# Kernel tuning notes

Measured on AMD Instinct MI355X. Metric: run time of the kernel, lower is better.

The kernel has to match this reference:

```python
import jax, jax.numpy as jnp
import numpy as np

N_NODES = 50000
N_EDGES = 800000
IN_DIM = 128
ATT_DIM = 128
NEG_SLOPE = 0.01  # nn.LeakyReLU default


def setup_inputs() -> dict:
    key = jax.random.key(0)
    ks = jax.random.split(key, 8)
    x = jax.random.normal(ks[0], (N_NODES, IN_DIM), dtype=jnp.float32)
    src_idx = jax.random.randint(ks[1], (N_EDGES,), 0, N_NODES, dtype=jnp.int32)
    dst_idx = jax.random.randint(ks[2], (N_EDGES,), 0, N_NODES, dtype=jnp.int32)
    # small init scale keeps exp(score) numerically tame
    src_w = jax.random.normal(ks[3], (IN_DIM, ATT_DIM), dtype=jnp.float32) * 0.05
    src_b = jnp.zeros((ATT_DIM,), dtype=jnp.float32)
    dst_w = jax.random.normal(ks[4], (IN_DIM, ATT_DIM), dtype=jnp.float32) * 0.05
    dst_b = jnp.zeros((ATT_DIM,), dtype=jnp.float32)
    att_w = jax.random.normal(ks[5], (ATT_DIM, 1), dtype=jnp.float32) * 0.05
    att_b = jnp.zeros((1,), dtype=jnp.float32)
    return {"x": x, "src_idx": src_idx, "dst_idx": dst_idx,
            "src_w": src_w, "src_b": src_b, "dst_w": dst_w, "dst_b": dst_b,
            "att_w": att_w, "att_b": att_b}


def reference(x, src_idx, dst_idx, src_w, src_b, dst_w, dst_b, att_w, att_b):
    n = x.shape[0]
    # 1) mean aggregation of source features onto destinations (copy_u + mean)
    deg = jax.ops.segment_sum(jnp.ones_like(dst_idx, dtype=x.dtype), dst_idx, num_segments=n)
    h_mean = jax.ops.segment_sum(x[src_idx], dst_idx, num_segments=n)
    h_mean = h_mean / jnp.maximum(deg, 1.0)[:, None]
    # 2) attention projections on nodes (dense GEMMs)
    ha_src = x @ src_w + src_b          # [N, att_dim]
    ha_dst = h_mean @ dst_w + dst_b     # [N, att_dim]
    # 3) per-edge u_add_v -> LeakyReLU -> att Linear -> exp
    e = jax.nn.leaky_relu(ha_src[src_idx] + ha_dst[dst_idx], NEG_SLOPE)  # [E, att_dim]
    s = jnp.exp(e @ att_w + att_b)      # [E, 1]
    # 4) edge softmax: normalize by segment sum over destination
    denom = jax.ops.segment_sum(s, dst_idx, num_segments=n)  # [N, 1]
    a = s / denom[dst_idx]              # [E, 1]
    # 5) u_mul_e weighted aggregation (sum)
    out = jax.ops.segment_sum(x[src_idx] * a, dst_idx, num_segments=n)  # [N, in_dim]
    return out
```

## Files before the change

kernel.cpp:

```cpp
#include <hip/hip_runtime.h>
#include <math.h>

#define N_NODES 50000
#define N_EDGES 800000
#define DIM 128
#define NEG_SLOPE 0.01f
#define CAP 64

#define SCAT_BLOCKS (N_EDGES / 256)
#define GEMM_BLOCKS ((N_NODES + 63) / 64)

typedef short v8s __attribute__((ext_vector_type(8)));
typedef float v4f __attribute__((ext_vector_type(4)));

__device__ inline unsigned f2bf2(float a, float b) {
    unsigned ua = __float_as_uint(a);
    unsigned ub = __float_as_uint(b);
    ua = (ua + 0x7fffu + ((ua >> 16) & 1u)) >> 16;
    ub = (ub + 0x7fffu + ((ub >> 16) & 1u)) & 0xffff0000u;
    return ua | ub;
}
__device__ inline float2 bf2f(unsigned u) {
    float2 r;
    r.x = __uint_as_float(u << 16);
    r.y = __uint_as_float(u & 0xffff0000u);
    return r;
}

__device__ inline float2 pka(float2 a, float2 b) {
    return make_float2(a.x + b.x, a.y + b.y);
}
__device__ inline float2 pkfma(float2 a, float2 b, float2 c) {
    return make_float2(fmaf(a.x, b.x, c.x), fmaf(a.y, b.y, c.y));
}
__device__ inline float2 leaky2(float2 v) {
    return make_float2(fmaxf(v.x, v.x * NEG_SLOPE), fmaxf(v.y, v.y * NEG_SLOPE));
}

#define ROR_ADD(v, CTRL) \
    ((v) + __int_as_float(__builtin_amdgcn_update_dpp( \
        0, __float_as_int(v), (CTRL), 0xf, 0xf, false)))

__global__ __launch_bounds__(256) void k_prepw(
    const float* __restrict__ src_w, const float* __restrict__ dst_w,
    unsigned* __restrict__ whT, int* __restrict__ deg)
{
    int gid = blockIdx.x * 256 + threadIdx.x;
    if (gid < 256 * 64) {
        int n = gid >> 6;
        int kk = gid & 63;
        const float* W = (n < 128) ? src_w : dst_w;
        int col = n & 127;
        float w0 = W[(2 * kk) * DIM + col];
        float w1 = W[(2 * kk + 1) * DIM + col];
        whT[gid] = f2bf2(w0, w1);
    }
    if (gid < N_NODES) deg[gid] = 0;
}

__global__ __launch_bounds__(256) void k_scatgemm(
    const int* __restrict__ src, const int* __restrict__ dst,
    int* __restrict__ deg, int* __restrict__ slots,
    const float* __restrict__ x, const unsigned* __restrict__ whT,
    const float* __restrict__ src_b, unsigned* __restrict__ hx_u,
    unsigned* __restrict__ yu)
{
    if (blockIdx.x < SCAT_BLOCKS) {
        int e = blockIdx.x * 256 + threadIdx.x;
        int d = dst[e];
        int pos = atomicAdd(&deg[d], 1);
        if (pos < CAP) slots[d * CAP + pos] = src[e] * 64;
        return;
    }

    __shared__ unsigned lds[64][196];
    int bx = blockIdx.x - SCAT_BLOCKS;
    int wave = threadIdx.x >> 6;
    int lane = threadIdx.x & 63;
    int quad = lane >> 4;
    int m = lane & 15;
    int m0 = bx * 64 + wave * 16;
    int arow = m0 + m;
    int lr = wave * 16 + m;
    bool live = (arow < N_NODES);

    v8s b[4];
    #pragma unroll
    for (int k0 = 0; k0 < 4; ++k0) {
        float4 f0 = make_float4(0.f, 0.f, 0.f, 0.f);
        float4 f1 = f0;
        if (live) {
            const float4* xp = (const float4*)(x + (size_t)arow * DIM + k0 * 32 + quad * 8);
            f0 = xp[0];
            f1 = xp[1];
        }
        union { unsigned u[4]; v8s s; } pk;
        pk.u[0] = f2bf2(f0.x, f0.y);
        pk.u[1] = f2bf2(f0.z, f0.w);
        pk.u[2] = f2bf2(f1.x, f1.y);
        pk.u[3] = f2bf2(f1.z, f1.w);
        b[k0] = pk.s;
        int c = k0 * 32 + quad * 8 + 1;
        lds[lr][c + 0] = pk.u[0];
        lds[lr][c + 2] = pk.u[1];
        lds[lr][c + 4] = pk.u[2];
        lds[lr][c + 6] = pk.u[3];
    }

    #pragma unroll
    for (int nt = 0; nt < 16; ++nt) {
        v4f acc = {0.f, 0.f, 0.f, 0.f};
        const uint4* ap = (const uint4*)(whT + (size_t)(nt * 16 + m) * 64 + quad * 4);
        #pragma unroll
        for (int k0 = 0; k0 < 4; ++k0) {
            union { uint4 u; v8s s; } af;
            af.u = ap[k0 * 4];
            acc = __builtin_amdgcn_mfma_f32_16x16x32_bf16(af.s, b[k0], acc, 0, 0, 0);
        }
        if (nt < 8) {
            float4 bia = ((const float4*)src_b)[nt * 4 + quad];
            int c = nt * 16 + quad * 4;
            lds[lr][c]     = f2bf2(acc[0] + bia.x, acc[1] + bia.y);
            lds[lr][c + 2] = f2bf2(acc[2] + bia.z, acc[3] + bia.w);
        } else {
            int c = 64 + nt * 8 + quad * 2;
            lds[lr][c]     = f2bf2(acc[0], acc[1]);
            lds[lr][c + 1] = f2bf2(acc[2], acc[3]);
        }
    }
    __syncthreads();

    int rbase = bx * 64;
    for (int i = threadIdx.x; i < 64 * 32; i += 256) {
        int r = i >> 5, c = i & 31;
        int row = rbase + r;
        if (row < N_NODES)
            ((uint4*)(hx_u + (size_t)row * 128))[c] = *(const uint4*)&lds[r][c * 4];
    }
    for (int i = threadIdx.x; i < 64 * 16; i += 256) {
        int r = i >> 4, c = i & 15;
        int row = rbase + r;
        if (row < N_NODES)
            ((uint4*)(yu + (size_t)row * 64))[c] = *(const uint4*)&lds[r][128 + c * 4];
    }
}

__global__ __launch_bounds__(256) void k_fuse(
    const uint2* __restrict__ hx, const unsigned* __restrict__ yu,
    const int* __restrict__ slots, const int* __restrict__ deg,
    const float* __restrict__ dst_b, const float* __restrict__ att_w,
    const float* __restrict__ att_b, float* __restrict__ out)
{
    int g = blockIdx.x * 256 + threadIdx.x;
    int node = g >> 6;
    int lane = g & 63;
    int grp = lane >> 4;
    int sl = lane & 15;
    int cnt = deg[node];
    if (cnt == 0) {
        if (grp < 2) {
            v4f z = {0.f, 0.f, 0.f, 0.f};
            __builtin_nontemporal_store(z, (v4f*)out + node * 32 + 2 * sl + grp);
        }
        return;
    }
    int cc = (cnt < CAP) ? cnt : CAP;
    int trips = (cc + 3) >> 2;
    int myoff = (lane < cc) ? slots[node * CAP + lane] : 0;

    float2 hd01 = {0.f, 0.f}, hd23 = {0.f, 0.f};
    float2 hd45 = {0.f, 0.f}, hd67 = {0.f, 0.f};
    #pragma unroll 2
    for (int t = 0; t < trips; ++t) {
        int i = 4 * t + grp;
        bool valid = (i < cc);
        int off = __shfl(myoff, valid ? i : 0);
        if (valid) {
            uint4 q = *((const uint4*)(yu + off) + sl);
            hd01 = pka(hd01, bf2f(q.x));
            hd23 = pka(hd23, bf2f(q.y));
            hd45 = pka(hd45, bf2f(q.z));
            hd67 = pka(hd67, bf2f(q.w));
        }
    }
    float inv = 1.0f / (float)cnt;
    float4 db0 = ((const float4*)dst_b)[2 * sl];
    float4 db1 = ((const float4*)dst_b)[2 * sl + 1];
    #define XRED(f) { f += __shfl_xor(f, 32); f += __shfl_xor(f, 16); f *= inv; }
    XRED(hd01.x) XRED(hd01.y) XRED(hd23.x) XRED(hd23.y)
    XRED(hd45.x) XRED(hd45.y) XRED(hd67.x) XRED(hd67.y)
    #undef XRED
    hd01.x += db0.x; hd01.y += db0.y; hd23.x += db0.z; hd23.y += db0.w;
    hd45.x += db1.x; hd45.y += db1.y; hd67.x += db1.z; hd67.y += db1.w;

    float4 aw0 = ((const float4*)att_w)[2 * sl];
    float4 aw1 = ((const float4*)att_w)[2 * sl + 1];
    float2 aw01 = make_float2(aw0.x, aw0.y), aw23 = make_float2(aw0.z, aw0.w);
    float2 aw45 = make_float2(aw1.x, aw1.y), aw67 = make_float2(aw1.z, aw1.w);
    float ab = att_b[0];
    float2 o01 = {0.f, 0.f}, o23 = {0.f, 0.f};
    float2 o45 = {0.f, 0.f}, o67 = {0.f, 0.f};
    float dsum = 0.f;
    #pragma unroll 2
    for (int t = 0; t < trips; ++t) {
        int i = 4 * t + grp;
        bool valid = (i < cc);
        int off = __shfl(myoff, valid ? i : 0);
        if (valid) {
            const uint4* hp = (const uint4*)(hx + off);
            uint4 qa = hp[2 * sl];
            uint4 qb = hp[2 * sl + 1];
            float2 p2 = {0.f, 0.f};
            p2 = pkfma(leaky2(pka(bf2f(qa.x), hd01)), aw01, p2);
            p2 = pkfma(leaky2(pka(bf2f(qa.z), hd23)), aw23, p2);
            p2 = pkfma(leaky2(pka(bf2f(qb.x), hd45)), aw45, p2);
            p2 = pkfma(leaky2(pka(bf2f(qb.z), hd67)), aw67, p2);
            float p = p2.x + p2.y;
            p = ROR_ADD(p, 0x128);
            p = ROR_ADD(p, 0x124);
            p = ROR_ADD(p, 0x122);
            p = ROR_ADD(p, 0x121);
            float s = __expf(p + ab);
            float2 s2 = make_float2(s, s);
            o01 = pkfma(bf2f(qa.y), s2, o01);
            o23 = pkfma(bf2f(qa.w), s2, o23);
            o45 = pkfma(bf2f(qb.y), s2, o45);
            o67 = pkfma(bf2f(qb.w), s2, o67);
            dsum += s;
        }
    }
    dsum += __shfl_xor(dsum, 32);
    dsum += __shfl_xor(dsum, 16);
    #define XRED2(f) { f += __shfl_xor(f, 32); f += __shfl_xor(f, 16); }
    XRED2(o01.x) XRED2(o01.y) XRED2(o23.x) XRED2(o23.y)
    XRED2(o45.x) XRED2(o45.y) XRED2(o67.x) XRED2(o67.y)
    #undef XRED2
    float r = 1.0f / dsum;
    if (grp < 2) {
        v4f ov;
        if (grp == 0) {
            ov[0] = o01.x * r; ov[1] = o01.y * r; ov[2] = o23.x * r; ov[3] = o23.y * r;
        } else {
            ov[0] = o45.x * r; ov[1] = o45.y * r; ov[2] = o67.x * r; ov[3] = o67.y * r;
        }
        __builtin_nontemporal_store(ov, (v4f*)out + node * 32 + 2 * sl + grp);
    }
}

extern "C" void kernel_launch(void* const* d_in, const int* in_sizes, int n_in,
                              void* d_out, int out_size, void* d_ws, size_t ws_size,
                              hipStream_t stream)
{
    const float* x     = (const float*)d_in[0];
    const int*   src   = (const int*)d_in[1];
    const int*   dst   = (const int*)d_in[2];
    const float* src_w = (const float*)d_in[3];
    const float* src_b = (const float*)d_in[4];
    const float* dst_w = (const float*)d_in[5];
    const float* dst_b = (const float*)d_in[6];
    const float* att_w = (const float*)d_in[7];
    const float* att_b = (const float*)d_in[8];
    float* out = (float*)d_out;
    (void)in_sizes; (void)n_in; (void)out_size; (void)ws_size;

    const size_t NF = (size_t)N_NODES * DIM;

    int* ws = (int*)d_ws;
    int* ideg  = ws;
    int* slots = ws + 50048;
    unsigned* whT = (unsigned*)(ws + 3250048);
    unsigned* yu  = whT + 16384;
    uint2*    hx  = (uint2*)(yu + NF / 2);

    k_prepw<<<256, 256, 0, stream>>>(src_w, dst_w, whT, ideg);

    k_scatgemm<<<SCAT_BLOCKS + GEMM_BLOCKS, 256, 0, stream>>>(
        src, dst, ideg, slots, x, whT, src_b, (unsigned*)hx, yu);

    k_fuse<<<N_NODES * 64 / 256, 256, 0, stream>>>(
        hx, yu, slots, ideg, dst_b, att_w, att_b, out);
}
```

Before: 256.7 us.

## Fold edge scatter into GEMM blocks to overlap atomics with MFMA work

Removes the separate scatter-only blocks and has each GEMM block process 1024 edges, prefetching src/dst indices up front and issuing the degree atomics and slot writes between the x load and the MFMA loop. This aims to hide atomic and index-load latency behind matrix compute and to cut the overhead of many short blocks. In exchange, each block does more serial work and holds more registers, and the grid is smaller.

```diff
diff --git a/kernel.cpp b/kernel.cpp
--- a/kernel.cpp
+++ b/kernel.cpp
@@ -7,8 +7,8 @@
 #define NEG_SLOPE 0.01f
 #define CAP 64
 
-#define SCAT_BLOCKS (N_EDGES / 256)
 #define GEMM_BLOCKS ((N_NODES + 63) / 64)
+#define EPB 1024
 
 typedef short v8s __attribute__((ext_vector_type(8)));
 typedef float v4f __attribute__((ext_vector_type(4)));
@@ -65,22 +65,25 @@
     const float* __restrict__ src_b, unsigned* __restrict__ hx_u,
     unsigned* __restrict__ yu)
 {
-    if (blockIdx.x < SCAT_BLOCKS) {
-        int e = blockIdx.x * 256 + threadIdx.x;
-        int d = dst[e];
-        int pos = atomicAdd(&deg[d], 1);
-        if (pos < CAP) slots[d * CAP + pos] = src[e] * 64;
-        return;
-    }
-
     __shared__ unsigned lds[64][196];
-    int bx = blockIdx.x - SCAT_BLOCKS;
-    int wave = threadIdx.x >> 6;
-    int lane = threadIdx.x & 63;
+    int bx = blockIdx.x;
+    int tid = threadIdx.x;
+
+    int e0 = bx * EPB + tid;
+    int sv[4], dv[4];
+    #pragma unroll
+    for (int i = 0; i < 4; ++i) {
+        int e = e0 + i * 256;
+        bool v = (e < N_EDGES);
+        sv[i] = v ? src[e] : 0;
+        dv[i] = v ? dst[e] : 0;
+    }
+
+    int wave = tid >> 6;
+    int lane = tid & 63;
     int quad = lane >> 4;
     int m = lane & 15;
-    int m0 = bx * 64 + wave * 16;
-    int arow = m0 + m;
+    int arow = bx * 64 + wave * 16 + m;
     int lr = wave * 16 + m;
     bool live = (arow < N_NODES);
 
@@ -108,6 +111,15 @@
     }
 
     #pragma unroll
+    for (int i = 0; i < 4; ++i) {
+        int e = e0 + i * 256;
+        if (e < N_EDGES) {
+            int pos = atomicAdd(&deg[dv[i]], 1);
+            if (pos < CAP) slots[dv[i] * CAP + pos] = sv[i] * 64;
+        }
+    }
+
+    #pragma unroll
     for (int nt = 0; nt < 16; ++nt) {
         v4f acc = {0.f, 0.f, 0.f, 0.f};
         const uint4* ap = (const uint4*)(whT + (size_t)(nt * 16 + m) * 64 + quad * 4);
@@ -131,13 +143,13 @@
     __syncthreads();
 
     int rbase = bx * 64;
-    for (int i = threadIdx.x; i < 64 * 32; i += 256) {
+    for (int i = tid; i < 64 * 32; i += 256) {
         int r = i >> 5, c = i & 31;
         int row = rbase + r;
         if (row < N_NODES)
             ((uint4*)(hx_u + (size_t)row * 128))[c] = *(const uint4*)&lds[r][c * 4];
     }
-    for (int i = threadIdx.x; i < 64 * 16; i += 256) {
+    for (int i = tid; i < 64 * 16; i += 256) {
         int r = i >> 4, c = i & 15;
         int row = rbase + r;
         if (row < N_NODES)
@@ -274,7 +286,7 @@
 
     k_prepw<<<256, 256, 0, stream>>>(src_w, dst_w, whT, ideg);
 
-    k_scatgemm<<<SCAT_BLOCKS + GEMM_BLOCKS, 256, 0, stream>>>(
+    k_scatgemm<<<GEMM_BLOCKS, 256, 0, stream>>>(
         src, dst, ideg, slots, x, whT, src_b, (unsigned*)hx, yu);
 
     k_fuse<<<N_NODES * 64 / 256, 256, 0, stream>>>(
```

New measurement: 253.2 us. Within noise of the previous version (-1.3%).
